# Optimization experiments

Measured on AMD Instinct MI355X. Metric: run time of the kernel, lower is better.

The kernel has to match this reference:

```python
import jax, jax.numpy as jnp
import numpy as np

NUM_USER = 20000
NUM_ITEM = 40000
N_NODES = NUM_USER + NUM_ITEM
DIM = 64
V_DIM = 2048
T_DIM = 768
N_EDGES = 1_000_000
K_USER = 40
K_ITEM = 10
N_LAYERS = 2


def setup_inputs() -> dict:
    key = jax.random.key(0)
    ks = iter(jax.random.split(key, 32))

    def xavier(shape):
        s = (2.0 / (shape[0] + shape[-1])) ** 0.5
        return jax.random.normal(next(ks), shape, jnp.float32) * s

    # bipartite user-item interactions, doubled (undirected), as in DRAGON.__init__
    u = jax.random.randint(next(ks), (N_EDGES,), 0, NUM_USER)
    it = jax.random.randint(next(ks), (N_EDGES,), NUM_USER, N_NODES)
    edge_index = jnp.stack([jnp.concatenate([u, it]), jnp.concatenate([it, u])])

    v_feat = jax.random.normal(next(ks), (NUM_ITEM, V_DIM), jnp.float32)
    t_feat = jax.random.normal(next(ks), (NUM_ITEM, T_DIM), jnp.float32)

    # KNN item-item adjacency (top-10 per row) with symmetric-normalized values,
    # mirroring get_knn_adj_mat/compute_normalized_laplacian
    rows = jnp.repeat(jnp.arange(NUM_ITEM), K_ITEM)
    cols = jax.random.randint(next(ks), (NUM_ITEM * K_ITEM,), 0, NUM_ITEM)
    mm_indices = jnp.stack([rows, cols])
    row_sum = jax.ops.segment_sum(jnp.ones(NUM_ITEM * K_ITEM, jnp.float32), rows,
                                  num_segments=NUM_ITEM) + 1e-7
    rinv = row_sum ** -0.5
    mm_values = rinv[rows] * rinv[cols]

    user_graph = jax.random.randint(next(ks), (NUM_USER, K_USER), 0, NUM_USER)
    user_weight_matrix = jax.nn.softmax(
        jax.random.normal(next(ks), (NUM_USER, K_USER), jnp.float32), axis=1)
    weight_u = jax.nn.softmax(
        jax.random.normal(next(ks), (NUM_USER, 2, 1), jnp.float32), axis=1)

    return {
        'edge_index': edge_index,
        'v_feat': v_feat, 't_feat': t_feat,
        'v_pref': xavier((NUM_USER, DIM)), 't_pref': xavier((NUM_USER, DIM)),
        'v_mlp1_w': xavier((V_DIM, 4 * DIM)), 'v_mlp1_b': jnp.zeros(4 * DIM, jnp.float32),
        'v_mlp2_w': xavier((4 * DIM, DIM)), 'v_mlp2_b': jnp.zeros(DIM, jnp.float32),
        't_mlp1_w': xavier((T_DIM, 4 * DIM)), 't_mlp1_b': jnp.zeros(4 * DIM, jnp.float32),
        't_mlp2_w': xavier((4 * DIM, DIM)), 't_mlp2_b': jnp.zeros(DIM, jnp.float32),
        'v_conv_w': xavier((DIM, DIM)), 'v_conv_b': jnp.zeros(DIM, jnp.float32),
        't_conv_w': xavier((DIM, DIM)), 't_conv_b': jnp.zeros(DIM, jnp.float32),
        'weight_u': weight_u,
        'user_graph': user_graph,
        'user_weight_matrix': user_weight_matrix,
        'mm_indices': mm_indices,
        'mm_values': mm_values,
    }


def _l2n(x):
    n = jnp.linalg.norm(x, axis=-1, keepdims=True)
    return x / jnp.maximum(n, 1e-12)


def reference(edge_index, v_feat, t_feat, v_pref, t_pref,
              v_mlp1_w, v_mlp1_b, v_mlp2_w, v_mlp2_b,
              t_mlp1_w, t_mlp1_b, t_mlp2_w, t_mlp2_b,
              v_conv_w, v_conv_b, t_conv_w, t_conv_b,
              weight_u, user_graph, user_weight_matrix,
              mm_indices, mm_values):
    seg = jax.ops.segment_sum
    # GCNConv normalization with self-loops (shared by both branches)
    sl = jnp.arange(N_NODES)
    src = jnp.concatenate([edge_index[0], sl])
    dst = jnp.concatenate([edge_index[1], sl])
    deg = seg(jnp.ones_like(dst, dtype=jnp.float32), dst, num_segments=N_NODES)
    dinv = deg ** -0.5
    norm = (dinv[src] * dinv[dst])[:, None]

    def conv(x, w, b):  # out[dst] += norm * (x @ w)[src], then bias
        return seg(norm * (x @ w)[src], dst, num_segments=N_NODES) + b

    def branch(feat, pref, w1, b1, w2, b2, cw, cb):
        temp = jax.nn.leaky_relu(feat @ w1 + b1) @ w2 + b2  # [I, D]
        x = _l2n(jnp.concatenate([pref, temp], axis=0))      # [N, D]
        h = conv(x, cw, cb)
        h1 = conv(h, cw, cb)
        return x + h + h1

    v_rep = branch(v_feat, v_pref, v_mlp1_w, v_mlp1_b, v_mlp2_w, v_mlp2_b, v_conv_w, v_conv_b)
    t_rep = branch(t_feat, t_pref, t_mlp1_w, t_mlp1_b, t_mlp2_w, t_mlp2_b, t_conv_w, t_conv_b)

    representation = jnp.concatenate([v_rep, t_rep], axis=1)  # [N, 2D]
    wu = weight_u[:, :, 0]  # [U, 2]
    user_rep = jnp.concatenate([wu[:, 0:1] * v_rep[:NUM_USER],
                                wu[:, 1:2] * t_rep[:NUM_USER]], axis=1)  # [U, 2D]
    item_rep = representation[NUM_USER:]  # [I, 2D]

    # User_Graph_sample: weighted sum over sampled user neighborhoods
    h_u = jnp.einsum('uk,ukd->ud', user_weight_matrix, user_rep[user_graph])
    user_rep = user_rep + h_u

    # n_layers of sparse Laplacian propagation over KNN item-item graph
    row, col = mm_indices[0], mm_indices[1]
    h_i = item_rep
    for _ in range(N_LAYERS):
        h_i = seg(mm_values[:, None] * h_i[col], row, num_segments=NUM_ITEM)
    item_rep = item_rep + h_i

    return jnp.concatenate([user_rep, item_rep], axis=0)  # [N, 2D]
```

## Files before the change

### kernel.cpp

```cpp
#include <hip/hip_runtime.h>

#define NUSER 20000
#define NITEM 40000
#define NNODE 60000
#define DIM   64
#define NE    1000000
#define KUSER 40
#define KITEM 10

typedef __attribute__((ext_vector_type(8))) short short8v;
typedef __attribute__((ext_vector_type(4))) float floatx4;

__device__ inline short bf16rne(float f) {
    unsigned u = __builtin_bit_cast(unsigned, f);
    unsigned r = (u + 0x7fffu + ((u >> 16) & 1u)) >> 16;
    return (short)r;
}
__device__ inline unsigned cvt_pk_bf16(float lo, float hi) {
    unsigned r;
    asm("v_cvt_pk_bf16_f32 %0, %1, %2" : "=v"(r) : "v"(lo), "v"(hi));
    return r;
}
__device__ inline float bflo(unsigned v) { return __builtin_bit_cast(float, v << 16); }
__device__ inline float bfhi(unsigned v) { return __builtin_bit_cast(float, v & 0xffff0000u); }

__global__ __launch_bounds__(256) void k_count(const int* __restrict__ dst, int* __restrict__ cnt, int n) {
    int i = blockIdx.x * 256 + threadIdx.x;
    if (i < n) atomicAdd(&cnt[dst[i]], 1);
}

__global__ __launch_bounds__(256) void k_dinv(const int* __restrict__ cnt, float* __restrict__ dinv) {
    int i = blockIdx.x * 256 + threadIdx.x;
    if (i < NNODE) dinv[i] = 1.0f / sqrtf((float)(cnt[i] + 1));
}

__global__ __launch_bounds__(256) void k_scanA(const int* __restrict__ v, int* __restrict__ excl,
                                               int* __restrict__ bsum, int n) {
    __shared__ int s[256];
    int t = threadIdx.x, i = blockIdx.x * 256 + t;
    int orig = (i < n) ? v[i] : 0;
    s[t] = orig; __syncthreads();
    #pragma unroll
    for (int off = 1; off < 256; off <<= 1) {
        int u = (t >= off) ? s[t - off] : 0;
        __syncthreads();
        s[t] += u;
        __syncthreads();
    }
    if (i < n) excl[i] = s[t] - orig;
    if (t == 255) bsum[blockIdx.x] = s[255];
}

__global__ __launch_bounds__(256) void k_scanB(int* __restrict__ bsum, int nb) {
    __shared__ int s[256];
    int t = threadIdx.x;
    int orig = (t < nb) ? bsum[t] : 0;
    s[t] = orig; __syncthreads();
    #pragma unroll
    for (int off = 1; off < 256; off <<= 1) {
        int u = (t >= off) ? s[t - off] : 0;
        __syncthreads();
        s[t] += u;
        __syncthreads();
    }
    if (t < nb) bsum[t] = s[t] - orig;
}

__global__ __launch_bounds__(256) void k_scanC(int* __restrict__ excl, const int* __restrict__ bsum,
                                               int* __restrict__ cursor, int n) {
    int i = blockIdx.x * 256 + threadIdx.x;
    if (i < n) {
        int v = excl[i] + bsum[blockIdx.x];
        excl[i] = v;
        cursor[i] = v;
    }
    if (i == 0) excl[n] = 2 * NE;
}

__global__ __launch_bounds__(256) void k_fill(const int* __restrict__ src, const int* __restrict__ dst,
                                              const float* __restrict__ dinv, int* __restrict__ cursor,
                                              unsigned* __restrict__ csr_pkd, int n) {
    int i = blockIdx.x * 256 + threadIdx.x;
    if (i >= n) return;
    int s = src[i], d = dst[i];
    unsigned pk = ((unsigned)(unsigned short)bf16rne(dinv[s]) << 16) | (unsigned)s;
    int pos = atomicAdd(&cursor[d], 1);
    csr_pkd[pos] = pk;
}

__global__ __launch_bounds__(256) void k_transpose_bf16(const float* __restrict__ B, short* __restrict__ Btb,
                                                        int K, int N) {
    __shared__ float s[16][17];
    int t = threadIdx.x, tx = t & 15, ty = t >> 4;
    int k0 = blockIdx.x * 16, n0 = blockIdx.y * 16;
    s[ty][tx] = B[(size_t)(k0 + ty) * N + n0 + tx];
    __syncthreads();
    int k = k0 + tx, n = n0 + ty;
    Btb[(size_t)(k >> 5) * (N * 32) + n * 32 + (k & 31)] = bf16rne(s[tx][ty]);
}

#define AP   40
#define MIDP 264
__global__ __launch_bounds__(256) void mlp_fused(const float* __restrict__ A, const short* __restrict__ B1t,
                                                 const float* __restrict__ b1, const short* __restrict__ B2t,
                                                 const float* __restrict__ b2, float* __restrict__ X, int K) {
    __shared__ short smem[2 * 64 * AP + 2 * 256 * AP];
    short* As = smem;
    short* Bs = smem + 2 * 64 * AP;
    const int tid = threadIdx.x;
    const int lane = tid & 63, wid = tid >> 6;
    const int rowBase = blockIdx.x * 64;

    const int sar = tid >> 2, sac = (tid & 3) * 8;
    const float* aptr = A + (size_t)(rowBase + sar) * K + sac;

    const int fk = (lane >> 4) * 8;
    const int faoff = (lane & 15) * AP + fk;
    const int fboff = (wid * 64 + (lane & 15)) * AP + fk;

    floatx4 acc[4][4];
    #pragma unroll
    for (int m = 0; m < 4; m++)
        #pragma unroll
        for (int n = 0; n < 4; n++) acc[m][n] = (floatx4)0.f;

    float4 ra0, ra1;
    short8v rb[4];
    const int nk = K >> 5;

    auto ldg = [&](int ks) {
        const float* ap = aptr + ks * 32;
        ra0 = *(const float4*)(ap);
        ra1 = *(const float4*)(ap + 4);
        const short* bsrc = B1t + (size_t)ks * 8192 + tid * 8;
        #pragma unroll
        for (int it = 0; it < 4; it++) rb[it] = *(const short8v*)(bsrc + it * 2048);
    };
    auto stv = [&](int buf) {
        uint4 av;
        av.x = cvt_pk_bf16(ra0.x, ra0.y); av.y = cvt_pk_bf16(ra0.z, ra0.w);
        av.z = cvt_pk_bf16(ra1.x, ra1.y); av.w = cvt_pk_bf16(ra1.z, ra1.w);
        *(uint4*)&As[buf * (64 * AP) + sar * AP + sac] = av;
        #pragma unroll
        for (int it = 0; it < 4; it++)
            *(short8v*)&Bs[buf * (256 * AP) + (sar + it * 64) * AP + sac] = rb[it];
    };

    ldg(0); stv(0);
    __syncthreads();
    int cur = 0;
    for (int ks = 0; ks < nk; ++ks) {
        if (ks + 1 < nk) ldg(ks + 1);
        short8v a[4], b[4];
        #pragma unroll
        for (int m = 0; m < 4; m++) a[m] = *(const short8v*)&As[cur * (64 * AP) + faoff + m * 16 * AP];
        #pragma unroll
        for (int n = 0; n < 4; n++) b[n] = *(const short8v*)&Bs[cur * (256 * AP) + fboff + n * 16 * AP];
        #pragma unroll
        for (int m = 0; m < 4; m++)
            #pragma unroll
            for (int n = 0; n < 4; n++)
                acc[m][n] = __builtin_amdgcn_mfma_f32_16x16x32_bf16(a[m], b[n], acc[m][n], 0, 0, 0);
        if (ks + 1 < nk) stv(cur ^ 1);
        __syncthreads();
        cur ^= 1;
    }

    short* mid = Bs;
    float bcol[4];
    #pragma unroll
    for (int n = 0; n < 4; n++) bcol[n] = b1[wid * 64 + n * 16 + (lane & 15)];
    #pragma unroll
    for (int m = 0; m < 4; m++)
        #pragma unroll
        for (int n = 0; n < 4; n++)
            #pragma unroll
            for (int q = 0; q < 4; q++) {
                int row = m * 16 + (lane >> 4) * 4 + q;
                int col = wid * 64 + n * 16 + (lane & 15);
                float v = acc[m][n][q] + bcol[n];
                v = v > 0.f ? v : 0.01f * v;
                mid[row * MIDP + col] = bf16rne(v);
            }
    __syncthreads();

    floatx4 acc2[4];
    #pragma unroll
    for (int n2 = 0; n2 < 4; n2++) acc2[n2] = (floatx4)0.f;
    const int arow = wid * 16 + (lane & 15);
    #pragma unroll
    for (int ks2 = 0; ks2 < 8; ++ks2) {
        short8v af = *(const short8v*)&mid[arow * MIDP + ks2 * 32 + fk];
        const short* bp = B2t + ks2 * 2048 + fk;
        short8v bf4[4];
        #pragma unroll
        for (int n2 = 0; n2 < 4; n2++) bf4[n2] = *(const short8v*)(bp + (n2 * 16 + (lane & 15)) * 32);
        #pragma unroll
        for (int n2 = 0; n2 < 4; n2++)
            acc2[n2] = __builtin_amdgcn_mfma_f32_16x16x32_bf16(af, bf4[n2], acc2[n2], 0, 0, 0);
    }

    float b2c[4];
    #pragma unroll
    for (int n2 = 0; n2 < 4; n2++) b2c[n2] = b2[n2 * 16 + (lane & 15)];
    #pragma unroll
    for (int q = 0; q < 4; ++q) {
        float v[4]; float ss = 0.f;
        #pragma unroll
        for (int n2 = 0; n2 < 4; n2++) { v[n2] = acc2[n2][q] + b2c[n2]; ss += v[n2] * v[n2]; }
        ss += __shfl_xor(ss, 1, 64);
        ss += __shfl_xor(ss, 2, 64);
        ss += __shfl_xor(ss, 4, 64);
        ss += __shfl_xor(ss, 8, 64);
        float sc = 1.f / fmaxf(sqrtf(ss), 1e-12f);
        int grow = rowBase + wid * 16 + (lane >> 4) * 4 + q;
        #pragma unroll
        for (int n2 = 0; n2 < 4; n2++)
            X[(size_t)grow * 64 + n2 * 16 + (lane & 15)] = v[n2] * sc;
    }
}

__global__ __launch_bounds__(256) void k_l2n_pref(const float* __restrict__ prefv, const float* __restrict__ preft,
                                                  float* __restrict__ xv, float* __restrict__ xt) {
    int row = blockIdx.x * 4 + (threadIdx.x >> 6);
    int lane = threadIdx.x & 63;
    if (row >= NUSER) return;
    const float* p = blockIdx.y ? preft : prefv;
    float* x = blockIdx.y ? xt : xv;
    float v = p[(size_t)row * 64 + lane];
    float ss = v * v;
    #pragma unroll
    for (int off = 32; off >= 1; off >>= 1) ss += __shfl_xor(ss, off, 64);
    x[(size_t)row * 64 + lane] = v / fmaxf(sqrtf(ss), 1e-12f);
}

__global__ __launch_bounds__(256) void conv_dual(const float* __restrict__ A0, const float* __restrict__ A1,
                                                 int lda, const float* __restrict__ Bv, const float* __restrict__ Bt2,
                                                 unsigned short* __restrict__ Ch) {
    __shared__ float As2[16][65];
    __shared__ float Bs2[16][65];
    const float* A = blockIdx.y ? A1 : A0;
    const float* B = blockIdx.y ? Bt2 : Bv;
    const int colOff = (int)blockIdx.y * 64;
    const int tid = threadIdx.x;
    const int tx = tid & 15, ty = tid >> 4;
    const int rowBase = blockIdx.x * 64;
    float acc[4][4] = {};
    for (int k0 = 0; k0 < 64; k0 += 16) {
        {
            int r = tid >> 2, c = (tid & 3) * 4;
            int gr = rowBase + r;
            float4 v = make_float4(0.f, 0.f, 0.f, 0.f);
            if (gr < NNODE) v = *(const float4*)(A + (size_t)gr * lda + k0 + c);
            As2[c + 0][r] = v.x; As2[c + 1][r] = v.y; As2[c + 2][r] = v.z; As2[c + 3][r] = v.w;
        }
        {
            int r = tid >> 4, c = (tid & 15) * 4;
            float4 v = *(const float4*)(B + (size_t)(k0 + r) * 64 + c);
            Bs2[r][c + 0] = v.x; Bs2[r][c + 1] = v.y; Bs2[r][c + 2] = v.z; Bs2[r][c + 3] = v.w;
        }
        __syncthreads();
        #pragma unroll
        for (int k = 0; k < 16; k++) {
            float a[4], b[4];
            #pragma unroll
            for (int i = 0; i < 4; i++) a[i] = As2[k][ty * 4 + i];
            #pragma unroll
            for (int j = 0; j < 4; j++) b[j] = Bs2[k][tx * 4 + j];
            #pragma unroll
            for (int i = 0; i < 4; i++)
                #pragma unroll
                for (int j = 0; j < 4; j++) acc[i][j] += a[i] * b[j];
        }
        __syncthreads();
    }
    const int gr0 = rowBase + ty * 4, gc = tx * 4;
    #pragma unroll
    for (int i = 0; i < 4; i++) {
        if (gr0 + i >= NNODE) break;
        uint2 hh;
        hh.x = cvt_pk_bf16(acc[i][0], acc[i][1]);
        hh.y = cvt_pk_bf16(acc[i][2], acc[i][3]);
        *(uint2*)(Ch + (size_t)(gr0 + i) * 128 + colOff + gc) = hh;
    }
}

__global__ __launch_bounds__(256) void k_gather2(const int* __restrict__ rowptr, const unsigned* __restrict__ csr_pkd,
                                                 const float* __restrict__ dinv, const unsigned* __restrict__ gw2,
                                                 const float* __restrict__ cbv, const float* __restrict__ cbt,
                                                 float* __restrict__ h2) {
    int row = blockIdx.x * 4 + (threadIdx.x >> 6);
    int lane = threadIdx.x & 63;
    if (row >= NNODE) return;
    int p0 = rowptr[row], p1 = rowptr[row + 1];
    float dr = dinv[row];
    unsigned sv = gw2[(size_t)row * 64 + lane];
    float ax0 = dr * bflo(sv), ay0 = dr * bfhi(sv);
    float ax1 = 0.f, ay1 = 0.f;
    for (int p = p0; p < p1; p += 64) {
        int c = p1 - p; if (c > 64) c = 64;
        unsigned pk = (lane < c) ? csr_pkd[p + lane] : 0u;
        int j = 0;
        for (; j + 4 <= c; j += 4) {
            unsigned e0 = __shfl(pk, j, 64),     e1 = __shfl(pk, j + 1, 64);
            unsigned e2 = __shfl(pk, j + 2, 64), e3 = __shfl(pk, j + 3, 64);
            unsigned v0 = gw2[(size_t)(e0 & 0xffffu) * 64 + lane];
            unsigned v1 = gw2[(size_t)(e1 & 0xffffu) * 64 + lane];
            unsigned v2 = gw2[(size_t)(e2 & 0xffffu) * 64 + lane];
            unsigned v3 = gw2[(size_t)(e3 & 0xffffu) * 64 + lane];
            float w0 = bfhi(e0), w1 = bfhi(e1), w2 = bfhi(e2), w3 = bfhi(e3);
            ax0 += w0 * bflo(v0); ay0 += w0 * bfhi(v0);
            ax1 += w1 * bflo(v1); ay1 += w1 * bfhi(v1);
            ax0 += w2 * bflo(v2); ay0 += w2 * bfhi(v2);
            ax1 += w3 * bflo(v3); ay1 += w3 * bfhi(v3);
        }
        for (; j < c; ++j) {
            unsigned e = __shfl(pk, j, 64);
            unsigned v = gw2[(size_t)(e & 0xffffu) * 64 + lane];
            float w = bfhi(e);
            ax0 += w * bflo(v); ay0 += w * bfhi(v);
        }
    }
    int c0 = 2 * lane;
    float b0 = (c0 < 64) ? cbv[c0] : cbt[c0 - 64];
    float b1 = (c0 + 1 < 64) ? cbv[c0 + 1] : cbt[c0 + 1 - 64];
    float2 r;
    r.x = b0 + dr * (ax0 + ax1);
    r.y = b1 + dr * (ay0 + ay1);
    *(float2*)(h2 + (size_t)row * 128 + c0) = r;
}

__global__ __launch_bounds__(256) void k_accum_rep(const float* __restrict__ xv, const float* __restrict__ xt,
                                                   const float* __restrict__ h2, const float* __restrict__ h12,
                                                   const float* __restrict__ weight_u, float* __restrict__ rep0) {
    int id = blockIdx.x * 256 + threadIdx.x;
    if (id >= NNODE * 128) return;
    int row = id >> 7, c = id & 127;
    const float* x = (c < 64) ? xv : xt;
    float s = x[(size_t)row * 64 + (c & 63)] + h2[id] + h12[id];
    float w = (row < NUSER) ? weight_u[row * 2 + (c >> 6)] : 1.0f;
    rep0[id] = w * s;
}

__global__ __launch_bounds__(256) void k_user(const float* __restrict__ rep0, const int* __restrict__ ug,
                                              const float* __restrict__ uwm, float* __restrict__ out) {
    int id = blockIdx.x * 256 + threadIdx.x;
    if (id >= NUSER * 128) return;
    int u = id >> 7, d = id & 127;
    float acc = rep0[id];
    #pragma unroll 4
    for (int k = 0; k < KUSER; k++) {
        int nb = ug[u * KUSER + k];
        acc += uwm[u * KUSER + k] * rep0[(size_t)nb * 128 + d];
    }
    out[id] = acc;
}

template<bool ADD_BASE>
__global__ __launch_bounds__(256) void k_item_prop(const float* __restrict__ srcrep, const int* __restrict__ col,
                                                   const float* __restrict__ vals, const float* __restrict__ base,
                                                   float* __restrict__ dstrep) {
    int id = blockIdx.x * 256 + threadIdx.x;
    if (id >= NITEM * 128) return;
    int r = id >> 7, d = id & 127;
    float acc = 0.f;
    #pragma unroll
    for (int j = 0; j < KITEM; j++) {
        int c = col[r * KITEM + j];
        acc += vals[r * KITEM + j] * srcrep[(size_t)c * 128 + d];
    }
    if (ADD_BASE) acc += base[id];
    dstrep[id] = acc;
}

extern "C" void kernel_launch(void* const* d_in, const int* in_sizes, int n_in,
                              void* d_out, int out_size, void* d_ws, size_t ws_size,
                              hipStream_t stream) {
    const int*   edge_index = (const int*)d_in[0];
    const float* v_feat   = (const float*)d_in[1];
    const float* t_feat   = (const float*)d_in[2];
    const float* v_pref   = (const float*)d_in[3];
    const float* t_pref   = (const float*)d_in[4];
    const float* v_mlp1_w = (const float*)d_in[5];
    const float* v_mlp1_b = (const float*)d_in[6];
    const float* v_mlp2_w = (const float*)d_in[7];
    const float* v_mlp2_b = (const float*)d_in[8];
    const float* t_mlp1_w = (const float*)d_in[9];
    const float* t_mlp1_b = (const float*)d_in[10];
    const float* t_mlp2_w = (const float*)d_in[11];
    const float* t_mlp2_b = (const float*)d_in[12];
    const float* v_conv_w = (const float*)d_in[13];
    const float* v_conv_b = (const float*)d_in[14];
    const float* t_conv_w = (const float*)d_in[15];
    const float* t_conv_b = (const float*)d_in[16];
    const float* weight_u = (const float*)d_in[17];
    const int*   user_graph = (const int*)d_in[18];
    const float* uwm      = (const float*)d_in[19];
    const int*   mm_indices = (const int*)d_in[20];
    const float* mm_values  = (const float*)d_in[21];
    float* out = (float*)d_out;

    char* wsb = (char*)d_ws;
    size_t off = 0;
    auto alloc = [&](size_t bytes) -> void* {
        void* p = wsb + off;
        off = (off + bytes + 255) & ~(size_t)255;
        return p;
    };
    int*      cnt     = (int*)     alloc(NNODE * 4);
    float*    dinv    = (float*)   alloc(NNODE * 4);
    int*      rowptr  = (int*)     alloc((NNODE + 1) * 4);
    int*      bsum    = (int*)     alloc(256 * 4);
    int*      cursor  = (int*)     alloc(NNODE * 4);
    unsigned* csr_pkd = (unsigned*)alloc((size_t)2 * NE * 4);
    short*    Btw     = (short*)   alloc((size_t)2048 * 256 * 2);
    short*    W2b     = (short*)   alloc((size_t)256 * 64 * 2);
    float*    xv      = (float*)   alloc((size_t)NNODE * DIM * 4);
    float*    xt      = (float*)   alloc((size_t)NNODE * DIM * 4);
    unsigned short* gw2 = (unsigned short*)alloc((size_t)NNODE * 128 * 2);
    float*    h2      = (float*)   alloc((size_t)NNODE * 128 * 4);
    float*    h12     = (float*)   alloc((size_t)NNODE * 128 * 4);
    float*    rep0    = (float*)   alloc((size_t)NNODE * 128 * 4);
    float*    tmp     = (float*)   alloc((size_t)NITEM * 128 * 4);
    (void)ws_size; (void)n_in; (void)in_sizes; (void)out_size;

    const int* e_src = edge_index;
    const int* e_dst = edge_index + 2 * NE;
    const int* mm_col = mm_indices + NITEM * KITEM;

    const int NB = (NNODE + 255) / 256;

    hipMemsetAsync(cnt, 0, NNODE * 4, stream);
    k_count<<<(2 * NE + 255) / 256, 256, 0, stream>>>(e_dst, cnt, 2 * NE);
    k_dinv<<<(NNODE + 255) / 256, 256, 0, stream>>>(cnt, dinv);
    k_scanA<<<NB, 256, 0, stream>>>(cnt, rowptr, bsum, NNODE);
    k_scanB<<<1, 256, 0, stream>>>(bsum, NB);
    k_scanC<<<NB, 256, 0, stream>>>(rowptr, bsum, cursor, NNODE);
    k_fill<<<(2 * NE + 255) / 256, 256, 0, stream>>>(e_src, e_dst, dinv, cursor, csr_pkd, 2 * NE);

    {
        dim3 t1(2048 / 16, 16);
        k_transpose_bf16<<<t1, 256, 0, stream>>>(v_mlp1_w, Btw, 2048, 256);
        dim3 t2(256 / 16, 4);
        k_transpose_bf16<<<t2, 256, 0, stream>>>(v_mlp2_w, W2b, 256, 64);
        mlp_fused<<<NITEM / 64, 256, 0, stream>>>(v_feat, Btw, v_mlp1_b, W2b, v_mlp2_b,
                                                  xv + (size_t)NUSER * DIM, 2048);
        dim3 t3(768 / 16, 16);
        k_transpose_bf16<<<t3, 256, 0, stream>>>(t_mlp1_w, Btw, 768, 256);
        k_transpose_bf16<<<t2, 256, 0, stream>>>(t_mlp2_w, W2b, 256, 64);
        mlp_fused<<<NITEM / 64, 256, 0, stream>>>(t_feat, Btw, t_mlp1_b, W2b, t_mlp2_b,
                                                  xt + (size_t)NUSER * DIM, 768);
    }
    {
        dim3 g(NUSER / 4, 2);
        k_l2n_pref<<<g, 256, 0, stream>>>(v_pref, t_pref, xv, xt);
    }

    {
        dim3 g((NNODE + 63) / 64, 2);
        conv_dual<<<g, 256, 0, stream>>>(xv, xt, DIM, v_conv_w, t_conv_w, gw2);
        k_gather2<<<(NNODE + 3) / 4, 256, 0, stream>>>(rowptr, csr_pkd, dinv, (const unsigned*)gw2,
                                                       v_conv_b, t_conv_b, h2);
        conv_dual<<<g, 256, 0, stream>>>(h2, h2 + 64, 128, v_conv_w, t_conv_w, gw2);
        k_gather2<<<(NNODE + 3) / 4, 256, 0, stream>>>(rowptr, csr_pkd, dinv, (const unsigned*)gw2,
                                                       v_conv_b, t_conv_b, h12);
    }

    k_accum_rep<<<(NNODE * 128 + 255) / 256, 256, 0, stream>>>(xv, xt, h2, h12, weight_u, rep0);

    k_user<<<(NUSER * 128 + 255) / 256, 256, 0, stream>>>(rep0, user_graph, uwm, out);

    const float* item0 = rep0 + (size_t)NUSER * 128;
    k_item_prop<false><<<(NITEM * 128 + 255) / 256, 256, 0, stream>>>(item0, mm_col, mm_values, nullptr, tmp);
    k_item_prop<true><<<(NITEM * 128 + 255) / 256, 256, 0, stream>>>(tmp, mm_col, mm_values, item0, out + (size_t)NUSER * 128);
}
```

Baseline: 661.8 us.

## Fuse second gather with rep accumulation and use bf16 copies for neighbor gathers

```diff
diff --git a/kernel.cpp b/kernel.cpp
--- a/kernel.cpp
+++ b/kernel.cpp
@@ -285,15 +285,9 @@
     }
 }
 
-__global__ __launch_bounds__(256) void k_gather2(const int* __restrict__ rowptr, const unsigned* __restrict__ csr_pkd,
-                                                 const float* __restrict__ dinv, const unsigned* __restrict__ gw2,
-                                                 const float* __restrict__ cbv, const float* __restrict__ cbt,
-                                                 float* __restrict__ h2) {
-    int row = blockIdx.x * 4 + (threadIdx.x >> 6);
-    int lane = threadIdx.x & 63;
-    if (row >= NNODE) return;
+__device__ inline float2 gather_row(const int* rowptr, const unsigned* csr_pkd, const unsigned* gw2,
+                                    int row, int lane, float dr) {
     int p0 = rowptr[row], p1 = rowptr[row + 1];
-    float dr = dinv[row];
     unsigned sv = gw2[(size_t)row * 64 + lane];
     float ax0 = dr * bflo(sv), ay0 = dr * bfhi(sv);
     float ax1 = 0.f, ay1 = 0.f;
@@ -321,56 +315,110 @@
             ax0 += w * bflo(v); ay0 += w * bfhi(v);
         }
     }
+    float2 r; r.x = ax0 + ax1; r.y = ay0 + ay1;
+    return r;
+}
+
+__global__ __launch_bounds__(256) void k_gather2(const int* __restrict__ rowptr, const unsigned* __restrict__ csr_pkd,
+                                                 const float* __restrict__ dinv, const unsigned* __restrict__ gw2,
+                                                 const float* __restrict__ cbv, const float* __restrict__ cbt,
+                                                 float* __restrict__ h2) {
+    int row = blockIdx.x * 4 + (threadIdx.x >> 6);
+    int lane = threadIdx.x & 63;
+    if (row >= NNODE) return;
+    float dr = dinv[row];
+    float2 g = gather_row(rowptr, csr_pkd, gw2, row, lane, dr);
     int c0 = 2 * lane;
     float b0 = (c0 < 64) ? cbv[c0] : cbt[c0 - 64];
     float b1 = (c0 + 1 < 64) ? cbv[c0 + 1] : cbt[c0 + 1 - 64];
     float2 r;
-    r.x = b0 + dr * (ax0 + ax1);
-    r.y = b1 + dr * (ay0 + ay1);
+    r.x = b0 + dr * g.x;
+    r.y = b1 + dr * g.y;
     *(float2*)(h2 + (size_t)row * 128 + c0) = r;
 }
 
-__global__ __launch_bounds__(256) void k_accum_rep(const float* __restrict__ xv, const float* __restrict__ xt,
-                                                   const float* __restrict__ h2, const float* __restrict__ h12,
-                                                   const float* __restrict__ weight_u, float* __restrict__ rep0) {
+__global__ __launch_bounds__(256) void k_gather2_rep(const int* __restrict__ rowptr, const unsigned* __restrict__ csr_pkd,
+                                                     const float* __restrict__ dinv, const unsigned* __restrict__ gw2,
+                                                     const float* __restrict__ cbv, const float* __restrict__ cbt,
+                                                     const float* __restrict__ xv, const float* __restrict__ xt,
+                                                     const float* __restrict__ h2, const float* __restrict__ weight_u,
+                                                     float* __restrict__ rep0, unsigned* __restrict__ rep_bf) {
+    int row = blockIdx.x * 4 + (threadIdx.x >> 6);
+    int lane = threadIdx.x & 63;
+    if (row >= NNODE) return;
+    float dr = dinv[row];
+    float2 g = gather_row(rowptr, csr_pkd, gw2, row, lane, dr);
+    int c0 = 2 * lane;
+    float b0 = (c0 < 64) ? cbv[c0] : cbt[c0 - 64];
+    float b1 = (c0 + 1 < 64) ? cbv[c0 + 1] : cbt[c0 + 1 - 64];
+    float h12x = b0 + dr * g.x;
+    float h12y = b1 + dr * g.y;
+    const float* x = (lane < 32) ? xv : xt;
+    float2 xp = *(const float2*)(x + (size_t)row * 64 + (c0 & 63));
+    float2 hp = *(const float2*)(h2 + (size_t)row * 128 + c0);
+    float w = (row < NUSER) ? weight_u[row * 2 + (lane >> 5)] : 1.0f;
+    float2 rp;
+    rp.x = w * (xp.x + hp.x + h12x);
+    rp.y = w * (xp.y + hp.y + h12y);
+    *(float2*)(rep0 + (size_t)row * 128 + c0) = rp;
+    rep_bf[(size_t)row * 64 + lane] = cvt_pk_bf16(rp.x, rp.y);
+}
+
+#define UBLK (NUSER * 64 / 256)
+__global__ __launch_bounds__(256) void k_user_item1(const float* __restrict__ rep0, const unsigned* __restrict__ rep_bf,
+                                                    const int* __restrict__ ug, const float* __restrict__ uwm,
+                                                    const int* __restrict__ mm_col, const float* __restrict__ mm_values,
+                                                    float* __restrict__ out, unsigned* __restrict__ tmp_bf) {
+    int bid = blockIdx.x;
+    if (bid < UBLK) {
+        int id = bid * 256 + threadIdx.x;
+        int u = id >> 6, lane = id & 63;
+        float2 acc = *(const float2*)(rep0 + (size_t)u * 128 + 2 * lane);
+        #pragma unroll 4
+        for (int k = 0; k < KUSER; k++) {
+            int nb = ug[u * KUSER + k];
+            float w = uwm[u * KUSER + k];
+            unsigned v = rep_bf[(size_t)nb * 64 + lane];
+            acc.x += w * bflo(v);
+            acc.y += w * bfhi(v);
+        }
+        *(float2*)(out + (size_t)u * 128 + 2 * lane) = acc;
+    } else {
+        int id = (bid - UBLK) * 256 + threadIdx.x;
+        int r = id >> 6, lane = id & 63;
+        float ax = 0.f, ay = 0.f;
+        #pragma unroll
+        for (int j = 0; j < KITEM; j++) {
+            int c = mm_col[r * KITEM + j];
+            float w = mm_values[r * KITEM + j];
+            unsigned v = rep_bf[(size_t)(NUSER + c) * 64 + lane];
+            ax += w * bflo(v);
+            ay += w * bfhi(v);
+        }
+        tmp_bf[(size_t)r * 64 + lane] = cvt_pk_bf16(ax, ay);
+    }
+}
+
+__global__ __launch_bounds__(256) void k_item2(const float* __restrict__ rep0, const unsigned* __restrict__ tmp_bf,
+                                               const int* __restrict__ mm_col, const float* __restrict__ mm_values,
+                                               float* __restrict__ out) {
     int id = blockIdx.x * 256 + threadIdx.x;
-    if (id >= NNODE * 128) return;
-    int row = id >> 7, c = id & 127;
-    const float* x = (c < 64) ? xv : xt;
-    float s = x[(size_t)row * 64 + (c & 63)] + h2[id] + h12[id];
-    float w = (row < NUSER) ? weight_u[row * 2 + (c >> 6)] : 1.0f;
-    rep0[id] = w * s;
-}
-
-__global__ __launch_bounds__(256) void k_user(const float* __restrict__ rep0, const int* __restrict__ ug,
-                                              const float* __restrict__ uwm, float* __restrict__ out) {
-    int id = blockIdx.x * 256 + threadIdx.x;
-    if (id >= NUSER * 128) return;
-    int u = id >> 7, d = id & 127;
-    float acc = rep0[id];
-    #pragma unroll 4
-    for (int k = 0; k < KUSER; k++) {
-        int nb = ug[u * KUSER + k];
-        acc += uwm[u * KUSER + k] * rep0[(size_t)nb * 128 + d];
-    }
-    out[id] = acc;
-}
-
-template<bool ADD_BASE>
-__global__ __launch_bounds__(256) void k_item_prop(const float* __restrict__ srcrep, const int* __restrict__ col,
-                                                   const float* __restrict__ vals, const float* __restrict__ base,
-                                                   float* __restrict__ dstrep) {
-    int id = blockIdx.x * 256 + threadIdx.x;
-    if (id >= NITEM * 128) return;
-    int r = id >> 7, d = id & 127;
-    float acc = 0.f;
+    int r = id >> 6, lane = id & 63;
+    if (r >= NITEM) return;
+    float ax = 0.f, ay = 0.f;
     #pragma unroll
     for (int j = 0; j < KITEM; j++) {
-        int c = col[r * KITEM + j];
-        acc += vals[r * KITEM + j] * srcrep[(size_t)c * 128 + d];
-    }
-    if (ADD_BASE) acc += base[id];
-    dstrep[id] = acc;
+        int c = mm_col[r * KITEM + j];
+        float w = mm_values[r * KITEM + j];
+        unsigned v = tmp_bf[(size_t)c * 64 + lane];
+        ax += w * bflo(v);
+        ay += w * bfhi(v);
+    }
+    float2 base = *(const float2*)(rep0 + (size_t)(NUSER + r) * 128 + 2 * lane);
+    float2 o;
+    o.x = base.x + ax;
+    o.y = base.y + ay;
+    *(float2*)(out + (size_t)(NUSER + r) * 128 + 2 * lane) = o;
 }
 
 extern "C" void kernel_launch(void* const* d_in, const int* in_sizes, int n_in,
@@ -419,9 +467,9 @@
     float*    xt      = (float*)   alloc((size_t)NNODE * DIM * 4);
     unsigned short* gw2 = (unsigned short*)alloc((size_t)NNODE * 128 * 2);
     float*    h2      = (float*)   alloc((size_t)NNODE * 128 * 4);
-    float*    h12     = (float*)   alloc((size_t)NNODE * 128 * 4);
     float*    rep0    = (float*)   alloc((size_t)NNODE * 128 * 4);
-    float*    tmp     = (float*)   alloc((size_t)NITEM * 128 * 4);
+    unsigned* rep_bf  = (unsigned*)alloc((size_t)NNODE * 64 * 4);
+    unsigned* tmp_bf  = (unsigned*)alloc((size_t)NITEM * 64 * 4);
     (void)ws_size; (void)n_in; (void)in_sizes; (void)out_size;
 
     const int* e_src = edge_index;
@@ -462,15 +510,12 @@
         k_gather2<<<(NNODE + 3) / 4, 256, 0, stream>>>(rowptr, csr_pkd, dinv, (const unsigned*)gw2,
                                                        v_conv_b, t_conv_b, h2);
         conv_dual<<<g, 256, 0, stream>>>(h2, h2 + 64, 128, v_conv_w, t_conv_w, gw2);
-        k_gather2<<<(NNODE + 3) / 4, 256, 0, stream>>>(rowptr, csr_pkd, dinv, (const unsigned*)gw2,
-                                                       v_conv_b, t_conv_b, h12);
-    }
-
-    k_accum_rep<<<(NNODE * 128 + 255) / 256, 256, 0, stream>>>(xv, xt, h2, h12, weight_u, rep0);
-
-    k_user<<<(NUSER * 128 + 255) / 256, 256, 0, stream>>>(rep0, user_graph, uwm, out);
-
-    const float* item0 = rep0 + (size_t)NUSER * 128;
-    k_item_prop<false><<<(NITEM * 128 + 255) / 256, 256, 0, stream>>>(item0, mm_col, mm_values, nullptr, tmp);
-    k_item_prop<true><<<(NITEM * 128 + 255) / 256, 256, 0, stream>>>(tmp, mm_col, mm_values, item0, out + (size_t)NUSER * 128);
-}
+        k_gather2_rep<<<(NNODE + 3) / 4, 256, 0, stream>>>(rowptr, csr_pkd, dinv, (const unsigned*)gw2,
+                                                           v_conv_b, t_conv_b, xv, xt, h2, weight_u,
+                                                           rep0, rep_bf);
+    }
+
+    k_user_item1<<<UBLK + NITEM * 64 / 256, 256, 0, stream>>>(rep0, rep_bf, user_graph, uwm,
+                                                              mm_col, mm_values, out, tmp_bf);
+    k_item2<<<NITEM * 64 / 256, 256, 0, stream>>>(rep0, tmp_bf, mm_col, mm_values, out);
+}
```

After: 600.2 us. -9.3%, faster.
